# Optimization experiments

Measured on AMD Instinct MI355X. Metric: run time of the kernel, lower is better.

## Reference

```python
import jax, jax.numpy as jnp
import numpy as np

BN_EPS = 1e-5
LEAKY_SLOPE = 0.2


def setup_inputs() -> dict:
    key = jax.random.key(0)
    k1, k2 = jax.random.split(key, 2)
    B, C, N, O, K = 8, 64, 4096, 64, 20
    x = jax.random.normal(k1, (B, C, N), dtype=jnp.float32)
    W = jax.random.normal(k2, (O, 2 * C), dtype=jnp.float32) * 0.05  # 1x1 conv weight
    gamma = jnp.ones((O,), dtype=jnp.float32)
    beta = jnp.zeros((O,), dtype=jnp.float32)
    return {"x": x, "W": W, "gamma": gamma, "beta": beta, "k": K}


def reference(x, W, gamma, beta, k):
    # x: (B, C, N)
    xt = jnp.transpose(x, (0, 2, 1))  # (B, N, C)
    # kNN via squared euclidean distances (same ordering as cdist p=2)
    sq = jnp.sum(xt * xt, axis=-1)  # (B, N)
    d2 = sq[:, :, None] + sq[:, None, :] - 2.0 * jnp.einsum('bnc,bmc->bnm', xt, xt)
    idx = jax.lax.top_k(-d2, k)[1]  # (B, N, k) nearest neighbors (incl. self)
    # gather neighbor features: (B, N, k, C)
    xj = jax.vmap(lambda f, i: f[i])(xt, idx)
    xi = xt[:, :, None, :]  # (B, N, 1, C)
    edge = jnp.concatenate([xj - xi, jnp.broadcast_to(xi, xj.shape)], axis=-1)  # (B, N, k, 2C)
    # 1x1 conv == channel GEMM
    h = jnp.einsum('bnkc,oc->bnko', edge, W)  # (B, N, k, O)
    # BatchNorm2d, training-mode batch statistics over (B, N, k) per channel
    mean = jnp.mean(h, axis=(0, 1, 2))
    var = jnp.mean(jnp.square(h - mean), axis=(0, 1, 2))
    hn = (h - mean) * jax.lax.rsqrt(var + BN_EPS) * gamma + beta
    # LeakyReLU(0.2); dropout omitted (eval / identity)
    act = jnp.where(hn >= 0, hn, LEAKY_SLOPE * hn)
    # max over the k neighbors -> (B, N, O) -> (B, O, N)
    out = jnp.max(act, axis=2)
    return jnp.transpose(out, (0, 2, 1))
```

## Files before the change

kernel.cpp:

```cpp
#include <hip/hip_runtime.h>
#include <math.h>

#define Bn 8
#define Cc 64
#define Nn 4096
#define Oo 64
#define Kk 20
#define Kh 10
#define QCAP 24
#define NTOT (Bn*Nn*Kk)

typedef __attribute__((ext_vector_type(8))) short short8;
typedef __attribute__((ext_vector_type(4))) float f32x4;

__device__ __forceinline__ unsigned bf16_rn(float v) {
  unsigned u = __float_as_uint(v);
  return (u + 0x7FFFu + ((u >> 16) & 1)) >> 16;
}

__device__ __forceinline__ float pair_swap_f(float v) {
  return __int_as_float(__builtin_amdgcn_mov_dpp(__float_as_int(v), 0xB1, 0xF, 0xF, true));
}
__device__ __forceinline__ int pair_swap_i(int v) {
  return __builtin_amdgcn_mov_dpp(v, 0xB1, 0xF, 0xF, true);
}

__device__ __forceinline__ void gload_lds16(const void* g, void* l) {
  __builtin_amdgcn_global_load_lds((const __attribute__((address_space(1))) void*)g,
                                   (__attribute__((address_space(3))) void*)l,
                                   16, 0, 0);
}

__global__ __launch_bounds__(256) void k_split(const float* __restrict__ x,
                                               unsigned short* __restrict__ xs3,
                                               float* __restrict__ sqv) {
  __shared__ float xs[64][68];
  int tid = threadIdx.x;
  int b = blockIdx.x & 7;
  int n0 = (blockIdx.x >> 3) << 6;
  for (int i = 0; i < 4; i++) {
    int c = i * 16 + (tid >> 4);
    int n = (tid & 15) * 4;
    float4 v = *(const float4*)&x[((size_t)b * Cc + c) * Nn + n0 + n];
    *(float4*)&xs[c][n] = v;
  }
  __syncthreads();
  for (int i = 0; i < 4; i++) {
    int n = i * 16 + (tid >> 4);
    int c = (tid & 15) * 4;
    ushort4 h4, m4, l4;
    unsigned short* hp = (unsigned short*)&h4;
    unsigned short* mp = (unsigned short*)&m4;
    unsigned short* lp = (unsigned short*)&l4;
#pragma unroll
    for (int j = 0; j < 4; j++) {
      float v = xs[c + j][n];
      unsigned hb = bf16_rn(v);
      float hf = __uint_as_float(hb << 16);
      float r1 = v - hf;
      unsigned mb = bf16_rn(r1);
      float mf = __uint_as_float(mb << 16);
      float r2 = r1 - mf;
      unsigned lb = bf16_rn(r2);
      hp[j] = (unsigned short)hb;
      mp[j] = (unsigned short)mb;
      lp[j] = (unsigned short)lb;
    }
    size_t o = ((size_t)(b << 12) + n0 + n) * 192 + c;
    *(ushort4*)&xs3[o] = h4;
    *(ushort4*)&xs3[o + 64] = m4;
    *(ushort4*)&xs3[o + 128] = l4;
  }
  if (tid < 64) {
    float s = 0.f;
#pragma unroll
    for (int c = 0; c < 64; c++) { float v = xs[c][tid]; s = fmaf(v, v, s); }
    sqv[b * Nn + n0 + tid] = s;
  }
}

__global__ __launch_bounds__(256) void k_y1z(const float* __restrict__ x,
                                             const float* __restrict__ Wm,
                                             float* __restrict__ y1,
                                             float* __restrict__ z) {
  __shared__ float xs[64][68];
  __shared__ float Wl[64][129];
  int tid = threadIdx.x;
  int b = blockIdx.x & 7;
  int n0 = (blockIdx.x >> 3) << 6;
  for (int i = tid; i < 64 * 128; i += 256) Wl[i >> 7][i & 127] = Wm[i];
  for (int i = 0; i < 4; i++) {
    int c = i * 16 + (tid >> 4);
    int n = (tid & 15) * 4;
    float4 v = *(const float4*)&x[((size_t)b * Cc + c) * Nn + n0 + n];
    *(float4*)&xs[c][n] = v;
  }
  __syncthreads();
  int o = tid & 63, ng = tid >> 6;
  for (int p = 0; p < 4; p++) {
    int nb = p * 16 + ng * 4;
    float a1[4] = {0.f, 0.f, 0.f, 0.f};
    float a2[4] = {0.f, 0.f, 0.f, 0.f};
#pragma unroll 8
    for (int c = 0; c < 64; c++) {
      float4 xv = *(const float4*)&xs[c][nb];
      float w1v = Wl[o][c], w2v = Wl[o][64 + c];
      float xa[4] = {xv.x, xv.y, xv.z, xv.w};
#pragma unroll
      for (int j = 0; j < 4; j++) {
        a1[j] = fmaf(xa[j], w1v, a1[j]);
        a2[j] = fmaf(xa[j], w2v, a2[j]);
      }
    }
#pragma unroll
    for (int j = 0; j < 4; j++) {
      size_t off = ((size_t)b * Nn + n0 + nb + j) * 64 + o;
      y1[off] = a1[j];
      z[off] = a2[j] - a1[j];
    }
  }
}

__global__ __launch_bounds__(512, 4) void k_knn(const unsigned short* __restrict__ xs3,
                                                const float* __restrict__ sqv,
                                                int* __restrict__ idxout) {
  __shared__ alignas(16) short Bs[2][12288];
  __shared__ alignas(16) float thrS[2][64];
  __shared__ alignas(16) float sqs[2][64];
  __shared__ alignas(16) float qk[2][64][QCAP];
  __shared__ alignas(16) unsigned short qm[2][64][QCAP];
  __shared__ int qcnt[2][64];

  const int tid = threadIdx.x;
  const int lane = tid & 63;
  const int w = tid >> 6;
  const int grp = w >> 2;
  const int wg = w & 3;
  const int tig = tid & 255;
  const int b = blockIdx.x & 7;
  const int n0 = (blockIdx.x >> 3) << 6;
  const int lm = lane & 15;
  const int q = lane >> 4;
  const bool handler = (lane < 32);
  const int hrow = wg * 16 + (lane >> 1);
  const bool isL = (lane & 1) == 0;
  const int rowq = wg * 16 + q * 4;

  float hk[Kh];
  int hix[Kh];
#pragma unroll
  for (int kk = 0; kk < Kh; kk++) { hk[kk] = INFINITY; hix[kk] = 0; }

  if (handler && !isL) { thrS[grp][hrow] = INFINITY; qcnt[grp][hrow] = 0; }

  const size_t arow = ((size_t)(b << 12) + n0 + wg * 16 + lm) * 192;
  short8 ah0 = *(const short8*)&xs3[arow + q * 8];
  short8 ah1 = *(const short8*)&xs3[arow + 32 + q * 8];
  short8 am0 = *(const short8*)&xs3[arow + 64 + q * 8];
  short8 am1 = *(const short8*)&xs3[arow + 96 + q * 8];
  short8 al0 = *(const short8*)&xs3[arow + 128 + q * 8];
  short8 al1 = *(const short8*)&xs3[arow + 160 + q * 8];

  const unsigned short* gbase = xs3 + ((size_t)(b << 12) + grp * 2048) * 192;
  int gofs[6];
  short* lbase[6];
#pragma unroll
  for (int i = 0; i < 6; i++) {
    int p = i * 256 + wg * 64 + lane;
    int gsrc = p ^ ((p / 24) & 7);
    gofs[i] = gsrc * 8;
    lbase[i] = &Bs[grp][(i * 256 + wg * 64) * 8];
  }
  const int qa = ((q ^ (lm & 7)) << 3);
  const int qb = (((q + 4) ^ (lm & 7)) << 3);
  const short* Bg = &Bs[grp][0];

  f32x4 acc[4];

  for (int t = 0; t < 32; t++) {
    const int m0 = grp * 2048 + t * 64;
    __syncthreads();
#pragma unroll
    for (int i = 0; i < 6; i++) gload_lds16(gbase + gofs[i], lbase[i]);
    if (tig < 16) gload_lds16(sqv + b * Nn + m0 + lane * 4, &sqs[grp][0]);
    gbase += 12288;
    __syncthreads();

#pragma unroll
    for (int g = 0; g < 4; g++) {
      const short* brow = Bg + (g * 16 + lm) * 192;
      short8 bh0 = *(const short8*)(brow + qa);
      short8 bh1 = *(const short8*)(brow + qb);
      short8 bm0 = *(const short8*)(brow + 64 + qa);
      short8 bm1 = *(const short8*)(brow + 64 + qb);
      short8 bl0 = *(const short8*)(brow + 128 + qa);
      short8 bl1 = *(const short8*)(brow + 128 + qb);
      f32x4 a = (f32x4){0.f, 0.f, 0.f, 0.f};
      a = __builtin_amdgcn_mfma_f32_16x16x32_bf16(am0, bm0, a, 0, 0, 0);
      a = __builtin_amdgcn_mfma_f32_16x16x32_bf16(am1, bm1, a, 0, 0, 0);
      a = __builtin_amdgcn_mfma_f32_16x16x32_bf16(ah0, bl0, a, 0, 0, 0);
      a = __builtin_amdgcn_mfma_f32_16x16x32_bf16(ah1, bl1, a, 0, 0, 0);
      a = __builtin_amdgcn_mfma_f32_16x16x32_bf16(al0, bh0, a, 0, 0, 0);
      a = __builtin_amdgcn_mfma_f32_16x16x32_bf16(al1, bh1, a, 0, 0, 0);
      a = __builtin_amdgcn_mfma_f32_16x16x32_bf16(ah0, bm0, a, 0, 0, 0);
      a = __builtin_amdgcn_mfma_f32_16x16x32_bf16(ah1, bm1, a, 0, 0, 0);
      a = __builtin_amdgcn_mfma_f32_16x16x32_bf16(am0, bh0, a, 0, 0, 0);
      a = __builtin_amdgcn_mfma_f32_16x16x32_bf16(am1, bh1, a, 0, 0, 0);
      a = __builtin_amdgcn_mfma_f32_16x16x32_bf16(ah0, bh0, a, 0, 0, 0);
      a = __builtin_amdgcn_mfma_f32_16x16x32_bf16(ah1, bh1, a, 0, 0, 0);
      acc[g] = a;
    }

    unsigned pend = 0;
    {
      float4 t4 = *(const float4*)&thrS[grp][rowq];
      float tl[4] = {t4.x, t4.y, t4.z, t4.w};
      if (grp) {
        float4 s4 = *(const float4*)&thrS[0][rowq];
        tl[0] = fminf(tl[0], s4.x); tl[1] = fminf(tl[1], s4.y);
        tl[2] = fminf(tl[2], s4.z); tl[3] = fminf(tl[3], s4.w);
      }
#pragma unroll
      for (int g = 0; g < 4; g++) {
        float sv = sqs[grp][g * 16 + lm];
#pragma unroll
        for (int r = 0; r < 4; r++) {
          float key = fmaf(-2.f, acc[g][r], sv);
          acc[g][r] = key;
          if (key < tl[r]) pend |= 1u << (g * 4 + r);
        }
      }
    }

    for (;;) {
      if (pend) {
#pragma unroll
        for (int g = 0; g < 4; g++) {
#pragma unroll
          for (int r = 0; r < 4; r++) {
            unsigned bit = 1u << (g * 4 + r);
            if (pend & bit) {
              int row = rowq + r;
              int p = atomicAdd(&qcnt[grp][row], 1);
              if (p < QCAP) {
                qk[grp][row][p] = acc[g][r];
                qm[grp][row][p] = (unsigned short)(m0 + g * 16 + lm);
                pend &= ~bit;
              }
            }
          }
        }
      }
      unsigned long long anyovf = __ballot(pend != 0);

      if (handler) {
        int cn = qcnt[grp][hrow];
        if (cn > QCAP) cn = QCAP;
        for (int p0 = 0; p0 < cn; p0 += 2) {
          float2 kv2 = *(const float2*)&qk[grp][hrow][p0];
          ushort2 mv2 = *(const ushort2*)&qm[grp][hrow][p0];
          float kva[2] = {kv2.x, kv2.y};
          unsigned short mva[2] = {mv2.x, mv2.y};
#pragma unroll
          for (int j = 0; j < 2; j++) {
            bool valid = (p0 + j < cn);
            float kv = kva[j];
            int ki = (int)mva[j];
            bool lins = kv < hk[Kh - 1];
            float pv_ = lins ? hk[Kh - 1] : kv;
            int pi_ = lins ? hix[Kh - 1] : ki;
            float rv = pair_swap_f(pv_);
            int ri = pair_swap_i(pi_);
            float mval = isL ? kv : rv;
            int midx = isL ? ki : ri;
            if (valid && mval < hk[Kh - 1]) {
              bool cm[Kh];
#pragma unroll
              for (int kk = 0; kk < Kh; kk++) cm[kk] = mval < hk[kk];
#pragma unroll
              for (int kk = Kh - 1; kk >= 1; kk--) {
                hk[kk]  = cm[kk] ? (cm[kk - 1] ? hk[kk - 1]  : mval) : hk[kk];
                hix[kk] = cm[kk] ? (cm[kk - 1] ? hix[kk - 1] : midx) : hix[kk];
              }
              if (cm[0]) { hk[0] = mval; hix[0] = midx; }
            }
          }
        }
        if (cn && !isL) { qcnt[grp][hrow] = 0; thrS[grp][hrow] = hk[Kh - 1]; }
      }
      if (!anyovf) break;
      if (pend) {
        float4 t4 = *(const float4*)&thrS[grp][rowq];
        float tl[4] = {t4.x, t4.y, t4.z, t4.w};
        if (grp) {
          float4 s4 = *(const float4*)&thrS[0][rowq];
          tl[0] = fminf(tl[0], s4.x); tl[1] = fminf(tl[1], s4.y);
          tl[2] = fminf(tl[2], s4.z); tl[3] = fminf(tl[3], s4.w);
        }
#pragma unroll
        for (int g = 0; g < 4; g++)
#pragma unroll
          for (int r = 0; r < 4; r++) {
            unsigned bit = 1u << (g * 4 + r);
            if ((pend & bit) && acc[g][r] >= tl[r]) pend &= ~bit;
          }
      }
    }
  }

  if (grp == 1 && handler) {
    int base = isL ? 0 : Kh;
#pragma unroll
    for (int kk = 0; kk < Kh; kk++) {
      qk[1][hrow][base + kk] = hk[kk];
      qm[1][hrow][base + kk] = (unsigned short)hix[kk];
    }
  }
  __syncthreads();
  if (grp == 0 && handler) {
    for (int p0 = 0; p0 < Kk; p0 += 4) {
      float4 kv4 = *(const float4*)&qk[1][hrow][p0];
      ushort4 mv4 = *(const ushort4*)&qm[1][hrow][p0];
      float kva[4] = {kv4.x, kv4.y, kv4.z, kv4.w};
      unsigned short mva[4] = {mv4.x, mv4.y, mv4.z, mv4.w};
#pragma unroll
      for (int j = 0; j < 4; j++) {
        float kv = kva[j];
        int ki = (int)mva[j];
        bool lins = kv < hk[Kh - 1];
        float pv_ = lins ? hk[Kh - 1] : kv;
        int pi_ = lins ? hix[Kh - 1] : ki;
        float rv = pair_swap_f(pv_);
        int ri = pair_swap_i(pi_);
        float mval = isL ? kv : rv;
        int midx = isL ? ki : ri;
        if (mval < hk[Kh - 1]) {
          bool cm[Kh];
#pragma unroll
          for (int kk = 0; kk < Kh; kk++) cm[kk] = mval < hk[kk];
#pragma unroll
          for (int kk = Kh - 1; kk >= 1; kk--) {
            hk[kk]  = cm[kk] ? (cm[kk - 1] ? hk[kk - 1]  : mval) : hk[kk];
            hix[kk] = cm[kk] ? (cm[kk - 1] ? hix[kk - 1] : midx) : hix[kk];
          }
          if (cm[0]) { hk[0] = mval; hix[0] = midx; }
        }
      }
    }
    size_t obase = ((size_t)b * Nn + n0 + hrow) * Kk + (isL ? 0 : Kh);
#pragma unroll
    for (int kk = 0; kk < Kh; kk++) idxout[obase + kk] = hix[kk];
  }
}

__global__ __launch_bounds__(256) void k_stats(const float* __restrict__ y1,
                                               const float* __restrict__ z,
                                               const int* __restrict__ idxp,
                                               float* __restrict__ parts) {
  __shared__ float rs[4][64];
  __shared__ float rq[4][64];
  int tid = threadIdx.x;
  int o = tid & 63, g = tid >> 6;
  int b = blockIdx.x & 7;
  int n0 = (blockIdx.x >> 3) << 6;
  const float* y1b = y1 + (size_t)b * Nn * 64;
  float s = 0.f, ss = 0.f;
  for (int t = 0; t < 16; t++) {
    int n = n0 + g + t * 4;
    size_t base = (size_t)b * Nn + n;
    float zv = z[base * 64 + o];
    const int* ip = idxp + base * Kk;
#pragma unroll
    for (int k = 0; k < Kk; k++) {
      int j = ip[k];
      float hv = y1b[(size_t)j * 64 + o] + zv;
      s += hv;
      ss = fmaf(hv, hv, ss);
    }
  }
  rs[g][o] = s;
  rq[g][o] = ss;
  __syncthreads();
  if (tid < 64) {
    parts[(size_t)blockIdx.x * 128 + tid] = rs[0][tid] + rs[1][tid] + rs[2][tid] + rs[3][tid];
    parts[(size_t)blockIdx.x * 128 + 64 + tid] = rq[0][tid] + rq[1][tid] + rq[2][tid] + rq[3][tid];
  }
}

__global__ __launch_bounds__(128) void k_reduce(const float* __restrict__ parts,
                                                float* __restrict__ stats) {
  int tid = threadIdx.x;
  float s = 0.f;
  for (int i = 0; i < 512; i += 4) {
    s += parts[(size_t)i * 128 + tid] + parts[(size_t)(i + 1) * 128 + tid] +
         parts[(size_t)(i + 2) * 128 + tid] + parts[(size_t)(i + 3) * 128 + tid];
  }
  stats[tid] = s;
}

__global__ __launch_bounds__(256) void k_out(const float* __restrict__ y1,
                                             const float* __restrict__ z,
                                             const int* __restrict__ idxp,
                                             const float* __restrict__ stats,
                                             const float* __restrict__ gamma,
                                             const float* __restrict__ beta,
                                             float* __restrict__ out) {
  __shared__ float T[64][65];
  int tid = threadIdx.x;
  int lane = tid & 63;
  int w = tid >> 6;
  int b = blockIdx.x & 7;
  int n0 = (blockIdx.x >> 3) << 6;
  int o = lane;
  const float inv = 1.0f / (float)NTOT;
  float mean = stats[o] * inv;
  float var = fmaf(-mean, mean, stats[64 + o] * inv);
  float sc = gamma[o] * rsqrtf(var + 1e-5f);
  float bi = fmaf(-mean, sc, beta[o]);
  const float* y1b = y1 + (size_t)b * Nn * 64;
  for (int t = 0; t < 16; t++) {
    int nl = w + t * 4;
    size_t base = (size_t)b * Nn + n0 + nl;
    float zv = z[base * 64 + o];
    const int* ip = idxp + base * Kk;
    float mv = -INFINITY;
#pragma unroll
    for (int k = 0; k < Kk; k++) {
      int j = ip[k];
      float hv = y1b[(size_t)j * 64 + o] + zv;
      float hn = fmaf(hv, sc, bi);
      float a = (hn >= 0.f) ? hn : 0.2f * hn;
      mv = fmaxf(mv, a);
    }
    T[o][nl] = mv;
  }
  __syncthreads();
  for (int t = 0; t < 16; t++) {
    int oo = w * 16 + t;
    out[((size_t)b * Oo + oo) * Nn + n0 + lane] = T[oo][lane];
  }
}

extern "C" void kernel_launch(void* const* d_in, const int* in_sizes, int n_in,
                              void* d_out, int out_size, void* d_ws, size_t ws_size,
                              hipStream_t stream) {
  const float* x = (const float*)d_in[0];
  const float* W = (const float*)d_in[1];
  const float* gamma = (const float*)d_in[2];
  const float* beta = (const float*)d_in[3];

  char* ws = (char*)d_ws;
  unsigned short* xs3 = (unsigned short*)ws;
  float* y1 = (float*)ws;
  float* z = (float*)(ws + 8388608);
  float* sq = (float*)(ws + 16777216);
  float* stats = (float*)(ws + 16908288);
  int* idx = (int*)(ws + 16908800);
  float* parts = (float*)(ws + 19530240);
  float* out = (float*)d_out;

  k_split<<<Bn * (Nn / 64), 256, 0, stream>>>(x, xs3, sq);
  k_knn<<<Bn * (Nn / 64), 512, 0, stream>>>(xs3, sq, idx);
  k_y1z<<<Bn * (Nn / 64), 256, 0, stream>>>(x, W, y1, z);
  k_stats<<<Bn * (Nn / 64), 256, 0, stream>>>(y1, z, idx, parts);
  k_reduce<<<1, 128, 0, stream>>>(parts, stats);
  k_out<<<Bn * (Nn / 64), 256, 0, stream>>>(y1, z, idx, stats, gamma, beta, out);
}
```

Measured before the change: 364.9 us.

## Double-buffer kNN candidate tiles and drop queue overflow retry loop

```diff
diff --git a/kernel.cpp b/kernel.cpp
--- a/kernel.cpp
+++ b/kernel.cpp
@@ -7,7 +7,7 @@
 #define Oo 64
 #define Kk 20
 #define Kh 10
-#define QCAP 24
+#define QCAP 32
 #define NTOT (Bn*Nn*Kk)
 
 typedef __attribute__((ext_vector_type(8))) short short8;
@@ -124,11 +124,11 @@
 __global__ __launch_bounds__(512, 4) void k_knn(const unsigned short* __restrict__ xs3,
                                                 const float* __restrict__ sqv,
                                                 int* __restrict__ idxout) {
-  __shared__ alignas(16) short Bs[2][12288];
+  __shared__ alignas(16) short Bs[2][2][6144];
   __shared__ alignas(16) float thrS[2][64];
-  __shared__ alignas(16) float sqs[2][64];
-  __shared__ alignas(16) float qk[2][64][QCAP];
-  __shared__ alignas(16) unsigned short qm[2][64][QCAP];
+  __shared__ alignas(16) float sqs[2][2][32];
+  __shared__ alignas(16) float qk[2][64][36];
+  __shared__ alignas(16) unsigned short qm[2][64][40];
   __shared__ int qcnt[2][64];
 
   const int tid = threadIdx.x;
@@ -162,32 +162,37 @@
   short8 al1 = *(const short8*)&xs3[arow + 160 + q * 8];
 
   const unsigned short* gbase = xs3 + ((size_t)(b << 12) + grp * 2048) * 192;
-  int gofs[6];
-  short* lbase[6];
-#pragma unroll
-  for (int i = 0; i < 6; i++) {
+  int gofs[3];
+  int lofs[3];
+#pragma unroll
+  for (int i = 0; i < 3; i++) {
     int p = i * 256 + wg * 64 + lane;
-    int gsrc = p ^ ((p / 24) & 7);
-    gofs[i] = gsrc * 8;
-    lbase[i] = &Bs[grp][(i * 256 + wg * 64) * 8];
+    gofs[i] = (p ^ ((p / 24) & 7)) * 8;
+    lofs[i] = (i * 256 + wg * 64) * 8;
   }
   const int qa = ((q ^ (lm & 7)) << 3);
   const int qb = (((q + 4) ^ (lm & 7)) << 3);
-  const short* Bg = &Bs[grp][0];
-
-  f32x4 acc[4];
-
-  for (int t = 0; t < 32; t++) {
-    const int m0 = grp * 2048 + t * 64;
+
+#pragma unroll
+  for (int i = 0; i < 3; i++) gload_lds16(gbase + gofs[i], &Bs[grp][0][lofs[i]]);
+  if (tig < 8) gload_lds16(sqv + b * Nn + grp * 2048 + lane * 4, &sqs[grp][0][0]);
+
+  int cur = 0;
+  for (int t = 0; t < 64; t++) {
+    const int m0 = grp * 2048 + t * 32;
     __syncthreads();
-#pragma unroll
-    for (int i = 0; i < 6; i++) gload_lds16(gbase + gofs[i], lbase[i]);
-    if (tig < 16) gload_lds16(sqv + b * Nn + m0 + lane * 4, &sqs[grp][0]);
-    gbase += 12288;
-    __syncthreads();
-
-#pragma unroll
-    for (int g = 0; g < 4; g++) {
+    if (t < 63) {
+      const unsigned short* gn = gbase + 6144;
+#pragma unroll
+      for (int i = 0; i < 3; i++) gload_lds16(gn + gofs[i], &Bs[grp][cur ^ 1][lofs[i]]);
+      if (tig < 8) gload_lds16(sqv + b * Nn + m0 + 32 + lane * 4, &sqs[grp][cur ^ 1][0]);
+      gbase = gn;
+    }
+
+    const short* Bg = &Bs[grp][cur][0];
+    f32x4 acc[2];
+#pragma unroll
+    for (int g = 0; g < 2; g++) {
       const short* brow = Bg + (g * 16 + lm) * 192;
       short8 bh0 = *(const short8*)(brow + qa);
       short8 bh1 = *(const short8*)(brow + qb);
@@ -221,8 +226,8 @@
         tl[2] = fminf(tl[2], s4.z); tl[3] = fminf(tl[3], s4.w);
       }
 #pragma unroll
-      for (int g = 0; g < 4; g++) {
-        float sv = sqs[grp][g * 16 + lm];
+      for (int g = 0; g < 2; g++) {
+        float sv = sqs[grp][cur][g * 16 + lm];
 #pragma unroll
         for (int r = 0; r < 4; r++) {
           float key = fmaf(-2.f, acc[g][r], sv);
@@ -232,80 +237,57 @@
       }
     }
 
-    for (;;) {
-      if (pend) {
-#pragma unroll
-        for (int g = 0; g < 4; g++) {
-#pragma unroll
-          for (int r = 0; r < 4; r++) {
-            unsigned bit = 1u << (g * 4 + r);
-            if (pend & bit) {
-              int row = rowq + r;
-              int p = atomicAdd(&qcnt[grp][row], 1);
-              if (p < QCAP) {
-                qk[grp][row][p] = acc[g][r];
-                qm[grp][row][p] = (unsigned short)(m0 + g * 16 + lm);
-                pend &= ~bit;
-              }
-            }
+    if (pend) {
+#pragma unroll
+      for (int g = 0; g < 2; g++) {
+#pragma unroll
+        for (int r = 0; r < 4; r++) {
+          unsigned bit = 1u << (g * 4 + r);
+          if (pend & bit) {
+            int row = rowq + r;
+            int p = atomicAdd(&qcnt[grp][row], 1);
+            qk[grp][row][p] = acc[g][r];
+            qm[grp][row][p] = (unsigned short)(m0 + g * 16 + lm);
           }
         }
       }
-      unsigned long long anyovf = __ballot(pend != 0);
-
-      if (handler) {
-        int cn = qcnt[grp][hrow];
-        if (cn > QCAP) cn = QCAP;
-        for (int p0 = 0; p0 < cn; p0 += 2) {
-          float2 kv2 = *(const float2*)&qk[grp][hrow][p0];
-          ushort2 mv2 = *(const ushort2*)&qm[grp][hrow][p0];
-          float kva[2] = {kv2.x, kv2.y};
-          unsigned short mva[2] = {mv2.x, mv2.y};
-#pragma unroll
-          for (int j = 0; j < 2; j++) {
-            bool valid = (p0 + j < cn);
-            float kv = kva[j];
-            int ki = (int)mva[j];
-            bool lins = kv < hk[Kh - 1];
-            float pv_ = lins ? hk[Kh - 1] : kv;
-            int pi_ = lins ? hix[Kh - 1] : ki;
-            float rv = pair_swap_f(pv_);
-            int ri = pair_swap_i(pi_);
-            float mval = isL ? kv : rv;
-            int midx = isL ? ki : ri;
-            if (valid && mval < hk[Kh - 1]) {
-              bool cm[Kh];
-#pragma unroll
-              for (int kk = 0; kk < Kh; kk++) cm[kk] = mval < hk[kk];
-#pragma unroll
-              for (int kk = Kh - 1; kk >= 1; kk--) {
-                hk[kk]  = cm[kk] ? (cm[kk - 1] ? hk[kk - 1]  : mval) : hk[kk];
-                hix[kk] = cm[kk] ? (cm[kk - 1] ? hix[kk - 1] : midx) : hix[kk];
-              }
-              if (cm[0]) { hk[0] = mval; hix[0] = midx; }
+    }
+
+    if (handler) {
+      int cn = qcnt[grp][hrow];
+      for (int p0 = 0; p0 < cn; p0 += 2) {
+        float2 kv2 = *(const float2*)&qk[grp][hrow][p0];
+        ushort2 mv2 = *(const ushort2*)&qm[grp][hrow][p0];
+        float kva[2] = {kv2.x, kv2.y};
+        unsigned short mva[2] = {mv2.x, mv2.y};
+#pragma unroll
+        for (int j = 0; j < 2; j++) {
+          bool valid = (p0 + j < cn);
+          float kv = kva[j];
+          int ki = (int)mva[j];
+          bool lins = kv < hk[Kh - 1];
+          float pv_ = lins ? hk[Kh - 1] : kv;
+          int pi_ = lins ? hix[Kh - 1] : ki;
+          float rv = pair_swap_f(pv_);
+          int ri = pair_swap_i(pi_);
+          float mval = isL ? kv : rv;
+          int midx = isL ? ki : ri;
+          if (valid && mval < hk[Kh - 1]) {
+            bool cm[Kh];
+#pragma unroll
+            for (int kk = 0; kk < Kh; kk++) cm[kk] = mval < hk[kk];
+#pragma unroll
+            for (int kk = Kh - 1; kk >= 1; kk--) {
+              hk[kk]  = cm[kk] ? (cm[kk - 1] ? hk[kk - 1]  : mval) : hk[kk];
+              hix[kk] = cm[kk] ? (cm[kk - 1] ? hix[kk - 1] : midx) : hix[kk];
             }
+            if (cm[0]) { hk[0] = mval; hix[0] = midx; }
           }
         }
-        if (cn && !isL) { qcnt[grp][hrow] = 0; thrS[grp][hrow] = hk[Kh - 1]; }
-      }
-      if (!anyovf) break;
-      if (pend) {
-        float4 t4 = *(const float4*)&thrS[grp][rowq];
-        float tl[4] = {t4.x, t4.y, t4.z, t4.w};
-        if (grp) {
-          float4 s4 = *(const float4*)&thrS[0][rowq];
-          tl[0] = fminf(tl[0], s4.x); tl[1] = fminf(tl[1], s4.y);
-          tl[2] = fminf(tl[2], s4.z); tl[3] = fminf(tl[3], s4.w);
-        }
-#pragma unroll
-        for (int g = 0; g < 4; g++)
-#pragma unroll
-          for (int r = 0; r < 4; r++) {
-            unsigned bit = 1u << (g * 4 + r);
-            if ((pend & bit) && acc[g][r] >= tl[r]) pend &= ~bit;
-          }
-      }
-    }
+      }
+      if (cn && !isL) { qcnt[grp][hrow] = 0; thrS[grp][hrow] = hk[Kh - 1]; }
+    }
+    cur ^= 1;
   }
 
   if (grp == 1 && handler) {
```

Result: no change. 366.6 us (+0.5%).
